# Kernel tuning notes

Hardware: AMD Instinct MI355X
Metric: run time of the kernel (lower is better)

The kernel has to match this reference:

```python
import jax, jax.numpy as jnp
import numpy as np

N = 500          # max_neurons, all alive
INPUT_SIZE = 3072
FEAT_DIM = 64
OUT_SIZE = 10
BATCH = 8192
RADIUS = 20.0
VOL = 100.0      # cubic volume (100,100,100)
N_ITER = 3


def setup_inputs() -> dict:
    key = jax.random.key(0)
    k_x, k_pos, k_iw, k_f, k_ow = jax.random.split(key, 5)
    x = jax.random.normal(k_x, (BATCH, INPUT_SIZE), dtype=jnp.float32)
    # seed positions spread across the volume, roughly matching _init_seeds
    positions = jax.random.uniform(k_pos, (N, 3), dtype=jnp.float32) * 80.0 + 10.0
    input_weights = jax.random.normal(k_iw, (N, INPUT_SIZE), dtype=jnp.float32) * 0.02
    features = jax.random.normal(k_f, (N, FEAT_DIM), dtype=jnp.float32) * 0.1
    output_weights = jax.random.normal(k_ow, (N, OUT_SIZE), dtype=jnp.float32) * 0.02
    biases = jnp.zeros((N,), dtype=jnp.float32)
    return {"x": x, "positions": positions, "input_weights": input_weights,
            "features": features, "output_weights": output_weights, "biases": biases}


def reference(x, positions, input_weights, features, output_weights, biases):
    # clamp positions into the volume (per-axis, vol is cubic here)
    pos = jnp.clip(positions, 0.1, VOL - 0.1)  # [N,3]

    # pairwise distances (grad-safe sqrt at the zero diagonal)
    diff = pos[:, None, :] - pos[None, :, :]          # [N,N,3]
    sq = jnp.sum(diff * diff, axis=-1)                # [N,N]
    pos_mask = sq > 0.0
    dist = jnp.where(pos_mask, jnp.sqrt(jnp.where(pos_mask, sq, 1.0)), 0.0)

    conn_mask = (dist < RADIUS) & (dist > 0.0)
    attenuation = jnp.exp(-dist / RADIUS) * conn_mask.astype(dist.dtype)

    # feature similarity (F.normalize clamps the norm from below at eps)
    feat_norm = features / jnp.maximum(
        jnp.linalg.norm(features, axis=1, keepdims=True), 1e-6)
    feat_sim = jnp.clip(feat_norm @ feat_norm.T, -1.0, 1.0)  # [N,N]

    conn_w = attenuation * (0.5 + 0.5 * feat_sim)
    conn_w = conn_w / (jnp.sum(conn_w, axis=1, keepdims=True) + 1e-6)

    # input gating: neurons near x=0 receive input
    x_norm = pos[:, 0] / VOL                          # [N]
    input_weight = jnp.exp(-2.0 * x_norm)
    input_weight = input_weight / (jnp.sum(input_weight) + 1e-6)

    activations = x @ input_weights.T * input_weight + biases  # [B,N]

    # iterative message passing (fixed small iteration count)
    for _ in range(N_ITER):
        msg = activations @ conn_w.T                  # [B,N]
        activations = jnp.minimum(jax.nn.relu(activations + 0.5 * msg), 50.0)

    # output gating: neurons near x=VOL emit output
    output_weight = jnp.exp(2.0 * (x_norm - 1.0))
    output_weight = output_weight / (jnp.sum(output_weight) + 1e-6)

    return activations @ (output_weights * output_weight[:, None])  # [B,OUT]
```

## Files before the change

### kernel.cpp

```cpp
#include <hip/hip_runtime.h>
#include <stdint.h>

#define N_REAL 500
#define NPAD   512
#define K_IN   3072
#define NBATCH 8192
#define NOUT   10
#define RADIUS 20.0f
#define VOLF   100.0f

typedef __attribute__((ext_vector_type(8))) __bf16 bf16x8;
typedef __attribute__((ext_vector_type(4))) float  f32x4;
typedef __attribute__((ext_vector_type(4))) unsigned short us4;

__device__ __forceinline__ unsigned short f2bf(float f) {
    unsigned int u = __float_as_uint(f);
    u += 0x7FFFu + ((u >> 16) & 1u);
    return (unsigned short)(u >> 16);
}
__device__ __forceinline__ float bf2f(unsigned short h) {
    return __uint_as_float(((unsigned int)h) << 16);
}
__device__ __forceinline__ uint2 cvt_pk4(float4 v) {
    uint2 r;
    asm("v_cvt_pk_bf16_f32 %0, %1, %2" : "=v"(r.x) : "v"(v.x), "v"(v.y));
    asm("v_cvt_pk_bf16_f32 %0, %1, %2" : "=v"(r.y) : "v"(v.z), "v"(v.w));
    return r;
}

#define GLOBAL_AS __attribute__((address_space(1)))
#define LDS_AS    __attribute__((address_space(3)))
__device__ __forceinline__ void glds16(const void* g, void* l) {
    __builtin_amdgcn_global_load_lds((const GLOBAL_AS void*)g, (LDS_AS void*)l, 16, 0, 0);
}

__global__ void prep1(const float* __restrict__ positions,
                      const float* __restrict__ features,
                      const float* __restrict__ out_w,
                      const float* __restrict__ biases,
                      float* __restrict__ feat_norm,
                      float* __restrict__ pos_c,
                      float* __restrict__ inw,
                      float* __restrict__ biasp,
                      float* __restrict__ wout)
{
    int n = threadIdx.x;
    float e_in = 0.f, e_out = 0.f;
    float px = 0.f, py = 0.f, pz = 0.f;
    if (n < N_REAL) {
        px = fminf(fmaxf(positions[n*3+0], 0.1f), VOLF - 0.1f);
        py = fminf(fmaxf(positions[n*3+1], 0.1f), VOLF - 0.1f);
        pz = fminf(fmaxf(positions[n*3+2], 0.1f), VOLF - 0.1f);
        float xn = px / VOLF;
        e_in  = expf(-2.f * xn);
        e_out = expf(2.f * (xn - 1.f));
        float ss = 0.f;
        for (int f = 0; f < 64; ++f) { float v = features[n*64+f]; ss += v*v; }
        float nm = fmaxf(sqrtf(ss), 1e-6f);
        for (int f = 0; f < 64; ++f) feat_norm[n*64+f] = features[n*64+f] / nm;
    } else {
        for (int f = 0; f < 64; ++f) feat_norm[n*64+f] = 0.f;
    }
    pos_c[n*4+0] = px; pos_c[n*4+1] = py; pos_c[n*4+2] = pz; pos_c[n*4+3] = 0.f;

    __shared__ float s_in[512], s_out[512];
    s_in[n] = e_in; s_out[n] = e_out;
    __syncthreads();
    for (int s = 256; s > 0; s >>= 1) {
        if (n < s) { s_in[n] += s_in[n+s]; s_out[n] += s_out[n+s]; }
        __syncthreads();
    }
    float sum_in  = s_in[0]  + 1e-6f;
    float sum_out = s_out[0] + 1e-6f;

    inw[n]   = (n < N_REAL) ? (e_in / sum_in) : 0.f;
    biasp[n] = (n < N_REAL) ? biases[n] : 0.f;
    float wo = (n < N_REAL) ? (e_out / sum_out) : 0.f;
    for (int o = 0; o < NOUT; ++o)
        wout[n*NOUT + o] = (n < N_REAL) ? out_w[n*NOUT + o] * wo : 0.f;
}

__global__ void prep2(const float* __restrict__ pos_c,
                      const float* __restrict__ feat_norm,
                      unsigned short* __restrict__ conn_w)
{
    int i = blockIdx.x;
    int t = threadIdx.x;
    __shared__ float fi[64];
    __shared__ float spos[4];
    __shared__ float red[128];
    if (t < 64) fi[t] = feat_norm[i*64 + t];
    if (t < 4)  spos[t] = pos_c[i*4 + t];
    __syncthreads();

    float w[4];
    float part = 0.f;
    for (int jj = 0; jj < 4; ++jj) {
        int j = t + jj*128;
        float val = 0.f;
        if (i < N_REAL && j < N_REAL) {
            float dx = spos[0] - pos_c[j*4+0];
            float dy = spos[1] - pos_c[j*4+1];
            float dz = spos[2] - pos_c[j*4+2];
            float sq = dx*dx + dy*dy + dz*dz;
            if (sq > 0.f) {
                float dist = sqrtf(sq);
                if (dist < RADIUS) {
                    float att = expf(-dist / RADIUS);
                    float sim = 0.f;
                    const float4* fj = (const float4*)(feat_norm + j*64);
                    const float4* fi4 = (const float4*)fi;
                    #pragma unroll
                    for (int f = 0; f < 16; ++f) {
                        float4 a = fi4[f]; float4 b = fj[f];
                        sim += a.x*b.x + a.y*b.y + a.z*b.z + a.w*b.w;
                    }
                    sim = fminf(fmaxf(sim, -1.f), 1.f);
                    val = att * (0.5f + 0.5f*sim);
                }
            }
        }
        w[jj] = val; part += val;
    }
    red[t] = part;
    __syncthreads();
    for (int s = 64; s > 0; s >>= 1) {
        if (t < s) red[t] += red[t+s];
        __syncthreads();
    }
    float inv = 1.f / (red[0] + 1e-6f);
    for (int jj = 0; jj < 4; ++jj)
        conn_w[(long)i*NPAD + t + jj*128] = f2bf(w[jj] * inv);
}

__global__ void cast_pad(const float* __restrict__ src, unsigned short* __restrict__ dst,
                         long total_q, long src_q)
{
    long i = (long)blockIdx.x * blockDim.x + threadIdx.x;
    long stride = (long)gridDim.x * blockDim.x;
    for (; i < total_q; i += stride) {
        us4 o;
        if (i < src_q) {
            float4 v = ((const float4*)src)[i];
            o[0] = f2bf(v.x); o[1] = f2bf(v.y); o[2] = f2bf(v.z); o[3] = f2bf(v.w);
        } else {
            o[0] = 0; o[1] = 0; o[2] = 0; o[3] = 0;
        }
        ((us4*)dst)[i] = o;
    }
}

__device__ __forceinline__ void block_map_g2(int b, int& m0, int& n0) {
    int xcd = b & 7, loc = b >> 3;
    m0 = (xcd*16 + (loc >> 2)) * 64;
    n0 = (loc & 3) * 128;
}

__global__ __launch_bounds__(256)
void gemm1_strict(const float* __restrict__ X,
                  const unsigned short* __restrict__ B,
                  unsigned short* __restrict__ Cbf,
                  const float* __restrict__ inw,
                  const float* __restrict__ biasp)
{
    __shared__ unsigned short As[64*64];
    __shared__ unsigned short Bs[128*64];

    const int tid  = threadIdx.x;
    const int lane = tid & 63;
    const int wave = tid >> 6;
    int m0, n0; block_map_g2(blockIdx.x, m0, n0);
    const int wm = (wave >> 1) * 32;
    const int wn = (wave & 1) * 64;

    f32x4 acc[2][4];
    #pragma unroll
    for (int i = 0; i < 2; ++i)
        #pragma unroll
        for (int j = 0; j < 4; ++j)
            acc[i][j] = (f32x4){0.f,0.f,0.f,0.f};

    const float4* gA[4]; int lAo[4];
    #pragma unroll
    for (int s = 0; s < 4; ++s) {
        int f = tid + s*256;
        int row = f >> 4, c4 = f & 15;
        gA[s] = (const float4*)(X + (long)(m0 + row) * K_IN) + c4;
        lAo[s] = row*128 + ((c4*8) ^ ((row & 7) << 4));
    }
    const char* gB[4]; char* lB[4];
    #pragma unroll
    for (int s = 0; s < 4; ++s) {
        int o = tid*16 + s*4096;
        int row = o >> 7, d = o & 127;
        gB[s] = (const char*)B + (long)(n0 + row) * (K_IN*2) + (d ^ ((row & 7) << 4));
        lB[s] = (char*)Bs + o;
    }

    for (int t = 0; t < 48; ++t) {
        __syncthreads();
        #pragma unroll
        for (int s = 0; s < 4; ++s) { glds16(gB[s], lB[s]); gB[s] += 128; }
        float4 v[4];
        #pragma unroll
        for (int s = 0; s < 4; ++s) { v[s] = gA[s][0]; gA[s] += 16; }
        #pragma unroll
        for (int s = 0; s < 4; ++s)
            *(uint2*)((char*)As + lAo[s]) = cvt_pk4(v[s]);
        asm volatile("s_waitcnt vmcnt(0) lgkmcnt(0)" ::: "memory");
        __syncthreads();

        #pragma unroll
        for (int kk = 0; kk < 2; ++kk) {
            const int cb = kk*64 + (lane >> 4) * 16;
            bf16x8 afr[2], bfr[4];
            #pragma unroll
            for (int i = 0; i < 2; ++i) {
                int r = wm + i*16 + (lane & 15);
                afr[i] = *(const bf16x8*)((const char*)As + r*128 + (cb ^ ((r & 7) << 4)));
            }
            #pragma unroll
            for (int j = 0; j < 4; ++j) {
                int r = wn + j*16 + (lane & 15);
                bfr[j] = *(const bf16x8*)((const char*)Bs + r*128 + (cb ^ ((r & 7) << 4)));
            }
            #pragma unroll
            for (int i = 0; i < 2; ++i)
                #pragma unroll
                for (int j = 0; j < 4; ++j)
                    acc[i][j] = __builtin_amdgcn_mfma_f32_16x16x32_bf16(afr[i], bfr[j], acc[i][j], 0, 0, 0);
        }
    }

    const int mbase = m0 + wm + (lane >> 4) * 4;
    const int nbase = n0 + wn + (lane & 15);
    #pragma unroll
    for (int j = 0; j < 4; ++j) {
        const int n = nbase + j*16;
        const float win = inw[n], bia = biasp[n];
        #pragma unroll
        for (int i = 0; i < 2; ++i)
            #pragma unroll
            for (int r = 0; r < 4; ++r) {
                const long m = mbase + i*16 + r;
                Cbf[m*NPAD + n] = f2bf(acc[i][j][r] * win + bia);
            }
    }
}

__global__ __launch_bounds__(256, 4)
void gemm2_pipe(const unsigned short* __restrict__ A,
                const unsigned short* __restrict__ B,
                unsigned short* __restrict__ Cbf,
                const unsigned short* __restrict__ actOld)
{
    constexpr int ABUF = 8192;
    constexpr int BBUF = 16384;
    __shared__ __align__(16) char lds[3*(ABUF+BBUF)];
    char* const Abase = lds;
    char* const Bbase = lds + 3*ABUF;

    const int tid  = threadIdx.x;
    const int lane = tid & 63;
    const int wave = tid >> 6;
    int m0, n0; block_map_g2(blockIdx.x, m0, n0);
    const int wm = (wave >> 1) * 32;
    const int wn = (wave & 1) * 64;

    f32x4 acc[2][4];
    #pragma unroll
    for (int i = 0; i < 2; ++i)
        #pragma unroll
        for (int j = 0; j < 4; ++j)
            acc[i][j] = (f32x4){0.f,0.f,0.f,0.f};

    const char* gB[4]; int lBo[4];
    #pragma unroll
    for (int s = 0; s < 4; ++s) {
        int o = tid*16 + s*4096;
        int row = o >> 7, d = o & 127;
        gB[s] = (const char*)B + (long)(n0 + row) * (NPAD*2) + (d ^ ((row & 7) << 4));
        lBo[s] = o;
    }
    const char* gA1[2]; int lAo1[2];
    #pragma unroll
    for (int s = 0; s < 2; ++s) {
        int o = tid*16 + s*4096;
        int row = o >> 7, d = o & 127;
        gA1[s] = (const char*)A + (long)(m0 + row) * (NPAD*2) + (d ^ ((row & 7) << 4));
        lAo1[s] = o;
    }

    const int NT = NPAD >> 6;

    #pragma unroll
    for (int s = 0; s < 2; ++s) { glds16(gA1[s], Abase + 0*ABUF + lAo1[s]); gA1[s] += 128; }
    #pragma unroll
    for (int s = 0; s < 4; ++s) { glds16(gB[s], Bbase + 0*BBUF + lBo[s]); gB[s] += 128; }
    #pragma unroll
    for (int s = 0; s < 2; ++s) { glds16(gA1[s], Abase + 1*ABUF + lAo1[s]); gA1[s] += 128; }
    #pragma unroll
    for (int s = 0; s < 4; ++s) { glds16(gB[s], Bbase + 1*BBUF + lBo[s]); gB[s] += 128; }

    int cur = 0;
    for (int t = 0; t < NT; ++t) {
        int fb = cur + 2; if (fb >= 3) fb -= 3;
        const bool more2 = (t + 2 < NT);
        const bool more1 = (t + 1 < NT);
        if (more2) {
            #pragma unroll
            for (int s = 0; s < 2; ++s) { glds16(gA1[s], Abase + fb*ABUF + lAo1[s]); gA1[s] += 128; }
            #pragma unroll
            for (int s = 0; s < 4; ++s) { glds16(gB[s], Bbase + fb*BBUF + lBo[s]); gB[s] += 128; }
            asm volatile("s_waitcnt vmcnt(12)" ::: "memory");
        } else if (more1) {
            asm volatile("s_waitcnt vmcnt(6)" ::: "memory");
        } else {
            asm volatile("s_waitcnt vmcnt(0)" ::: "memory");
        }
        __builtin_amdgcn_s_barrier();

        const char* Ab = Abase + cur*ABUF;
        const char* Bb = Bbase + cur*BBUF;
        #pragma unroll
        for (int kk = 0; kk < 2; ++kk) {
            const int cb = kk*64 + (lane >> 4) * 16;
            bf16x8 afr[2], bfr[4];
            #pragma unroll
            for (int i = 0; i < 2; ++i) {
                int r = wm + i*16 + (lane & 15);
                afr[i] = *(const bf16x8*)(Ab + r*128 + (cb ^ ((r & 7) << 4)));
            }
            #pragma unroll
            for (int j = 0; j < 4; ++j) {
                int r = wn + j*16 + (lane & 15);
                bfr[j] = *(const bf16x8*)(Bb + r*128 + (cb ^ ((r & 7) << 4)));
            }
            #pragma unroll
            for (int i = 0; i < 2; ++i)
                #pragma unroll
                for (int j = 0; j < 4; ++j)
                    acc[i][j] = __builtin_amdgcn_mfma_f32_16x16x32_bf16(afr[i], bfr[j], acc[i][j], 0, 0, 0);
        }
        __builtin_amdgcn_s_barrier();
        cur = (cur == 2) ? 0 : cur + 1;
    }

    const int mbase = m0 + wm + (lane >> 4) * 4;
    const int nbase = n0 + wn + (lane & 15);
    #pragma unroll
    for (int j = 0; j < 4; ++j) {
        const int n = nbase + j*16;
        #pragma unroll
        for (int i = 0; i < 2; ++i)
            #pragma unroll
            for (int r = 0; r < 4; ++r) {
                const long m = mbase + i*16 + r;
                float old = bf2f(actOld[m*NPAD + n]);
                float vv = fminf(fmaxf(old + 0.5f * acc[i][j][r], 0.f), 50.f);
                Cbf[m*NPAD + n] = f2bf(vv);
            }
    }
}

__global__ __launch_bounds__(256)
void out_gemm(const unsigned short* __restrict__ act,
              const float* __restrict__ wout,
              float* __restrict__ out)
{
    __shared__ float sw[NPAD * NOUT];
    const int tid = threadIdx.x;
    for (int i = tid; i < NPAD*NOUT; i += 256) sw[i] = wout[i];
    __syncthreads();

    const int lane = tid & 63;
    const int wv   = tid >> 6;
    const int row  = blockIdx.x * 4 + wv;

    const unsigned short* ap = act + (long)row * NPAD + lane * 8;
    us4 v0 = *(const us4*)(ap);
    us4 v1 = *(const us4*)(ap + 4);

    float p[NOUT];
    #pragma unroll
    for (int o = 0; o < NOUT; ++o) p[o] = 0.f;

    const int nb = lane * 8;
    #pragma unroll
    for (int e = 0; e < 8; ++e) {
        float a = bf2f(e < 4 ? v0[e] : v1[e-4]);
        const float* wr = &sw[(nb + e) * NOUT];
        #pragma unroll
        for (int o = 0; o < NOUT; ++o) p[o] += a * wr[o];
    }
    #pragma unroll
    for (int o = 0; o < NOUT; ++o) {
        float s = p[o];
        for (int d = 32; d > 0; d >>= 1) s += __shfl_down(s, d);
        if (lane == 0) out[(long)row * NOUT + o] = s;
    }
}

extern "C" void kernel_launch(void* const* d_in, const int* in_sizes, int n_in,
                              void* d_out, int out_size, void* d_ws, size_t ws_size,
                              hipStream_t stream)
{
    const float* x        = (const float*)d_in[0];
    const float* pos      = (const float*)d_in[1];
    const float* in_w     = (const float*)d_in[2];
    const float* feats    = (const float*)d_in[3];
    const float* out_w    = (const float*)d_in[4];
    const float* biases   = (const float*)d_in[5];
    float* out = (float*)d_out;

    char* ws = (char*)d_ws;
    unsigned short* iw_bf  = (unsigned short*)(ws);
    unsigned short* connw  = (unsigned short*)(ws + 3145728);
    unsigned short* act_a  = (unsigned short*)(ws + 3670016);
    unsigned short* act_b  = (unsigned short*)(ws + 12058624);
    float* feat_norm = (float*)(ws + 20447232);
    float* pos_c     = (float*)(ws + 20578304);
    float* inw       = (float*)(ws + 20586496);
    float* biasp     = (float*)(ws + 20588544);
    float* wout      = (float*)(ws + 20590592);

    prep1<<<1, 512, 0, stream>>>(pos, feats, out_w, biases, feat_norm, pos_c, inw, biasp, wout);
    prep2<<<512, 128, 0, stream>>>(pos_c, feat_norm, connw);
    cast_pad<<<512, 256, 0, stream>>>(in_w, iw_bf, 393216L, 384000L);

    gemm1_strict<<<512, 256, 0, stream>>>(x, iw_bf, act_a, inw, biasp);

    gemm2_pipe<<<512, 256, 0, stream>>>(act_a, connw, act_b, act_a);
    gemm2_pipe<<<512, 256, 0, stream>>>(act_b, connw, act_a, act_b);
    gemm2_pipe<<<512, 256, 0, stream>>>(act_a, connw, act_b, act_a);

    out_gemm<<<NBATCH/4, 256, 0, stream>>>(act_b, wout, out);
}
```

Baseline: 116.1 us.

## Fuse output projection into last message-passing GEMM and merge cast into prep

The final message-passing GEMM now applies the output projection in its epilogue. It writes per-column-tile partial outputs to a workspace, and a small combine kernel sums the four partials. This avoids writing and re-reading the final activation matrix. The bf16 cast of the input weights is folded into the prep1 launch as extra blocks, removing one kernel launch. The cost is a heavier epilogue with LDS staging and cross-lane shuffles, plus an extra tiny kernel.

```diff
diff --git a/kernel.cpp b/kernel.cpp
--- a/kernel.cpp
+++ b/kernel.cpp
@@ -34,16 +34,36 @@
     __builtin_amdgcn_global_load_lds((const GLOBAL_AS void*)g, (LDS_AS void*)l, 16, 0, 0);
 }
 
-__global__ void prep1(const float* __restrict__ positions,
-                      const float* __restrict__ features,
-                      const float* __restrict__ out_w,
-                      const float* __restrict__ biases,
-                      float* __restrict__ feat_norm,
-                      float* __restrict__ pos_c,
-                      float* __restrict__ inw,
-                      float* __restrict__ biasp,
-                      float* __restrict__ wout)
-{
+__global__ void prep1_cast(const float* __restrict__ positions,
+                           const float* __restrict__ features,
+                           const float* __restrict__ out_w,
+                           const float* __restrict__ biases,
+                           const float* __restrict__ iw_src,
+                           float* __restrict__ feat_norm,
+                           float* __restrict__ pos_c,
+                           float* __restrict__ inw,
+                           float* __restrict__ biasp,
+                           float* __restrict__ wout,
+                           unsigned short* __restrict__ iw_bf)
+{
+    __shared__ float s_in[512], s_out[512];
+    if (blockIdx.x != 0) {
+        const long total_q = 393216L, src_q = 384000L;
+        long i = (long)(blockIdx.x - 1) * 512 + threadIdx.x;
+        const long stride = 512L * 512L;
+        for (; i < total_q; i += stride) {
+            us4 o;
+            if (i < src_q) {
+                float4 v = ((const float4*)iw_src)[i];
+                o[0] = f2bf(v.x); o[1] = f2bf(v.y); o[2] = f2bf(v.z); o[3] = f2bf(v.w);
+            } else {
+                o[0] = 0; o[1] = 0; o[2] = 0; o[3] = 0;
+            }
+            ((us4*)iw_bf)[i] = o;
+        }
+        return;
+    }
+
     int n = threadIdx.x;
     float e_in = 0.f, e_out = 0.f;
     float px = 0.f, py = 0.f, pz = 0.f;
@@ -63,7 +83,6 @@
     }
     pos_c[n*4+0] = px; pos_c[n*4+1] = py; pos_c[n*4+2] = pz; pos_c[n*4+3] = 0.f;
 
-    __shared__ float s_in[512], s_out[512];
     s_in[n] = e_in; s_out[n] = e_out;
     __syncthreads();
     for (int s = 256; s > 0; s >>= 1) {
@@ -133,23 +152,6 @@
         conn_w[(long)i*NPAD + t + jj*128] = f2bf(w[jj] * inv);
 }
 
-__global__ void cast_pad(const float* __restrict__ src, unsigned short* __restrict__ dst,
-                         long total_q, long src_q)
-{
-    long i = (long)blockIdx.x * blockDim.x + threadIdx.x;
-    long stride = (long)gridDim.x * blockDim.x;
-    for (; i < total_q; i += stride) {
-        us4 o;
-        if (i < src_q) {
-            float4 v = ((const float4*)src)[i];
-            o[0] = f2bf(v.x); o[1] = f2bf(v.y); o[2] = f2bf(v.z); o[3] = f2bf(v.w);
-        } else {
-            o[0] = 0; o[1] = 0; o[2] = 0; o[3] = 0;
-        }
-        ((us4*)dst)[i] = o;
-    }
-}
-
 __device__ __forceinline__ void block_map_g2(int b, int& m0, int& n0) {
     int xcd = b & 7, loc = b >> 3;
     m0 = (xcd*16 + (loc >> 2)) * 64;
@@ -248,11 +250,14 @@
     }
 }
 
+template<int FUSE_OUT>
 __global__ __launch_bounds__(256, 4)
 void gemm2_pipe(const unsigned short* __restrict__ A,
                 const unsigned short* __restrict__ B,
                 unsigned short* __restrict__ Cbf,
-                const unsigned short* __restrict__ actOld)
+                const unsigned short* __restrict__ actOld,
+                const float* __restrict__ wout_g,
+                float* __restrict__ qout)
 {
     constexpr int ABUF = 8192;
     constexpr int BBUF = 16384;
@@ -348,57 +353,83 @@
 
     const int mbase = m0 + wm + (lane >> 4) * 4;
     const int nbase = n0 + wn + (lane & 15);
-    #pragma unroll
-    for (int j = 0; j < 4; ++j) {
-        const int n = nbase + j*16;
-        #pragma unroll
-        for (int i = 0; i < 2; ++i)
-            #pragma unroll
-            for (int r = 0; r < 4; ++r) {
-                const long m = mbase + i*16 + r;
-                float old = bf2f(actOld[m*NPAD + n]);
-                float vv = fminf(fmaxf(old + 0.5f * acc[i][j][r], 0.f), 50.f);
-                Cbf[m*NPAD + n] = f2bf(vv);
-            }
+
+    if (FUSE_OUT == 0) {
+        #pragma unroll
+        for (int j = 0; j < 4; ++j) {
+            const int n = nbase + j*16;
+            #pragma unroll
+            for (int i = 0; i < 2; ++i)
+                #pragma unroll
+                for (int r = 0; r < 4; ++r) {
+                    const long m = mbase + i*16 + r;
+                    float old = bf2f(actOld[m*NPAD + n]);
+                    float vv = fminf(fmaxf(old + 0.5f * acc[i][j][r], 0.f), 50.f);
+                    Cbf[m*NPAD + n] = f2bf(vv);
+                }
+        }
+    } else {
+        #pragma unroll
+        for (int j = 0; j < 4; ++j) {
+            const int n = nbase + j*16;
+            #pragma unroll
+            for (int i = 0; i < 2; ++i)
+                #pragma unroll
+                for (int r = 0; r < 4; ++r) {
+                    const long m = mbase + i*16 + r;
+                    float old = bf2f(actOld[m*NPAD + n]);
+                    acc[i][j][r] = fminf(fmaxf(old + 0.5f * acc[i][j][r], 0.f), 50.f);
+                }
+        }
+        float* swout = (float*)lds;
+        float* xw    = (float*)(lds + 20480);
+        for (int e = tid; e < NPAD*NOUT; e += 256) swout[e] = wout_g[e];
+        __builtin_amdgcn_s_barrier();
+
+        const int rlocal = wm + (lane >> 4) * 4;
+        #pragma unroll 1
+        for (int o = 0; o < NOUT; ++o) {
+            float po[8];
+            #pragma unroll
+            for (int i = 0; i < 2; ++i)
+                #pragma unroll
+                for (int r = 0; r < 4; ++r) {
+                    float s = 0.f;
+                    #pragma unroll
+                    for (int j = 0; j < 4; ++j)
+                        s += acc[i][j][r] * swout[(nbase + j*16)*NOUT + o];
+                    po[i*4+r] = s;
+                }
+            #pragma unroll
+            for (int d = 1; d < 16; d <<= 1)
+                #pragma unroll
+                for (int p = 0; p < 8; ++p)
+                    po[p] += __shfl_xor(po[p], d);
+            if ((lane & 15) == 0) {
+                #pragma unroll
+                for (int i = 0; i < 2; ++i)
+                    #pragma unroll
+                    for (int r = 0; r < 4; ++r)
+                        xw[(wave & 1)*640 + (rlocal + i*16 + r)*NOUT + o] = po[i*4+r];
+            }
+        }
+        __builtin_amdgcn_s_barrier();
+        const int q = n0 >> 7;
+        for (int e = tid; e < 64*NOUT; e += 256) {
+            int row = e / NOUT, o = e % NOUT;
+            float val = xw[row*NOUT + o] + xw[640 + row*NOUT + o];
+            qout[(long)q * (NBATCH*NOUT) + (long)(m0 + row)*NOUT + o] = val;
+        }
     }
 }
 
 __global__ __launch_bounds__(256)
-void out_gemm(const unsigned short* __restrict__ act,
-              const float* __restrict__ wout,
-              float* __restrict__ out)
-{
-    __shared__ float sw[NPAD * NOUT];
-    const int tid = threadIdx.x;
-    for (int i = tid; i < NPAD*NOUT; i += 256) sw[i] = wout[i];
-    __syncthreads();
-
-    const int lane = tid & 63;
-    const int wv   = tid >> 6;
-    const int row  = blockIdx.x * 4 + wv;
-
-    const unsigned short* ap = act + (long)row * NPAD + lane * 8;
-    us4 v0 = *(const us4*)(ap);
-    us4 v1 = *(const us4*)(ap + 4);
-
-    float p[NOUT];
-    #pragma unroll
-    for (int o = 0; o < NOUT; ++o) p[o] = 0.f;
-
-    const int nb = lane * 8;
-    #pragma unroll
-    for (int e = 0; e < 8; ++e) {
-        float a = bf2f(e < 4 ? v0[e] : v1[e-4]);
-        const float* wr = &sw[(nb + e) * NOUT];
-        #pragma unroll
-        for (int o = 0; o < NOUT; ++o) p[o] += a * wr[o];
-    }
-    #pragma unroll
-    for (int o = 0; o < NOUT; ++o) {
-        float s = p[o];
-        for (int d = 32; d > 0; d >>= 1) s += __shfl_down(s, d);
-        if (lane == 0) out[(long)row * NOUT + o] = s;
-    }
+void out_combine(const float* __restrict__ qout, float* __restrict__ out)
+{
+    const int TOT = NBATCH * NOUT;
+    int i = blockIdx.x * 256 + threadIdx.x;
+    if (i < TOT)
+        out[i] = ((qout[i] + qout[TOT + i]) + qout[2*TOT + i]) + qout[3*TOT + i];
 }
 
 extern "C" void kernel_launch(void* const* d_in, const int* in_sizes, int n_in,
@@ -423,16 +454,17 @@
     float* inw       = (float*)(ws + 20586496);
     float* biasp     = (float*)(ws + 20588544);
     float* wout      = (float*)(ws + 20590592);
-
-    prep1<<<1, 512, 0, stream>>>(pos, feats, out_w, biases, feat_norm, pos_c, inw, biasp, wout);
+    float* qout      = (float*)(ws + 20611072);
+
+    prep1_cast<<<513, 512, 0, stream>>>(pos, feats, out_w, biases, in_w,
+                                        feat_norm, pos_c, inw, biasp, wout, iw_bf);
     prep2<<<512, 128, 0, stream>>>(pos_c, feat_norm, connw);
-    cast_pad<<<512, 256, 0, stream>>>(in_w, iw_bf, 393216L, 384000L);
 
     gemm1_strict<<<512, 256, 0, stream>>>(x, iw_bf, act_a, inw, biasp);
 
-    gemm2_pipe<<<512, 256, 0, stream>>>(act_a, connw, act_b, act_a);
-    gemm2_pipe<<<512, 256, 0, stream>>>(act_b, connw, act_a, act_b);
-    gemm2_pipe<<<512, 256, 0, stream>>>(act_a, connw, act_b, act_a);
-
-    out_gemm<<<NBATCH/4, 256, 0, stream>>>(act_b, wout, out);
-}
+    gemm2_pipe<0><<<512, 256, 0, stream>>>(act_a, connw, act_b, act_a, nullptr, nullptr);
+    gemm2_pipe<0><<<512, 256, 0, stream>>>(act_b, connw, act_a, act_b, nullptr, nullptr);
+    gemm2_pipe<1><<<512, 256, 0, stream>>>(act_a, connw, nullptr, act_a, wout, qout);
+
+    out_combine<<<(NBATCH*NOUT + 255)/256, 256, 0, stream>>>(qout, out);
+}
```

New measurement: 110.7 us. 1.05x faster.
